# Kernel tuning notes

Hardware: AMD Instinct MI355X
Metric: run time of the kernel (lower is better)

## Reference

```python
import math
import jax, jax.numpy as jnp
import numpy as np

B, T, C, H = 4, 2048, 1024, 16
HD = C // H

def gelu_tanh(x):
    return 0.5 * x * (1.0 + jnp.tanh(jnp.sqrt(2.0 / jnp.pi) * (x + 0.044715 * x * x * x)))

def layernorm(x, w, b, eps=1e-5):
    mu = jnp.mean(x, axis=-1, keepdims=True)
    var = jnp.var(x, axis=-1, keepdims=True)
    return (x - mu) * jax.lax.rsqrt(var + eps) * w + b

def setup_inputs() -> dict:
    key = jax.random.key(0)
    ks = jax.random.split(key, 8)
    s = 0.02
    return {
        "x": jax.random.normal(ks[0], (B, T, C), dtype=jnp.float32),
        "ln1_w": jnp.ones((C,), jnp.float32), "ln1_b": jnp.zeros((C,), jnp.float32),
        "attn_w": jax.random.normal(ks[1], (C, 3 * C), jnp.float32) * s,
        "attn_b": jnp.zeros((3 * C,), jnp.float32),
        "proj_w": jax.random.normal(ks[2], (C, C), jnp.float32) * s,
        "proj_b": jnp.zeros((C,), jnp.float32),
        "ln2_w": jnp.ones((C,), jnp.float32), "ln2_b": jnp.zeros((C,), jnp.float32),
        "fc_w": jax.random.normal(ks[3], (C, 4 * C), jnp.float32) * s,
        "fc_b": jnp.zeros((4 * C,), jnp.float32),
        "fc_proj_w": jax.random.normal(ks[4], (4 * C, C), jnp.float32) * s,
        "fc_proj_b": jnp.zeros((C,), jnp.float32),
    }

def block(x, ln1_w, ln1_b, attn_w, attn_b, proj_w, proj_b,
          ln2_w, ln2_b, fc_w, fc_b, fc_proj_w, fc_proj_b):
    # --- causal self-attention ---
    h = layernorm(x, ln1_w, ln1_b)
    qkv = h @ attn_w + attn_b                      # [B,T,3C]
    q, k, v = jnp.split(qkv, 3, axis=-1)
    q = q.reshape(B, T, H, HD).transpose(0, 2, 1, 3)  # [B,H,T,hd]
    k = k.reshape(B, T, H, HD).transpose(0, 2, 1, 3)
    v = v.reshape(B, T, H, HD).transpose(0, 2, 1, 3)
    att = jnp.einsum('bhqd,bhkd->bhqk', q, k) * (1.0 / math.sqrt(HD))
    mask = jnp.tril(jnp.ones((T, T), dtype=bool))
    att = jnp.where(mask, att, -jnp.inf)
    att = jax.nn.softmax(att, axis=-1)
    y = jnp.einsum('bhqk,bhkd->bhqd', att, v)
    y = y.transpose(0, 2, 1, 3).reshape(B, T, C)
    x = x + (y @ proj_w + proj_b)
    # --- MLP ---
    h = layernorm(x, ln2_w, ln2_b)
    h = gelu_tanh(h @ fc_w + fc_b)
    x = x + (h @ fc_proj_w + fc_proj_b)
    return x

def reference(x, ln1_w, ln1_b, attn_w, attn_b, proj_w, proj_b,
              ln2_w, ln2_b, fc_w, fc_b, fc_proj_w, fc_proj_b):
    return block(x, ln1_w, ln1_b, attn_w, attn_b, proj_w, proj_b,
                 ln2_w, ln2_b, fc_w, fc_b, fc_proj_w, fc_proj_b)
```

## Files before the change

### kernel.cpp

```cpp
#include <hip/hip_runtime.h>
#include <stdint.h>

#define TSEQ 2048
#define CDIM 1024
#define NHEAD 16
#define HDIM 64
#define NROWS 8192

typedef __bf16 bf16x8 __attribute__((ext_vector_type(8)));
typedef float f32x4 __attribute__((ext_vector_type(4)));
typedef float f32x16 __attribute__((ext_vector_type(16)));

__device__ __forceinline__ unsigned short f2bf(float f) {
  unsigned u = __builtin_bit_cast(unsigned, f);
  u = u + 0x7fffu + ((u >> 16) & 1u);
  return (unsigned short)(u >> 16);
}

__device__ __forceinline__ unsigned cvt_pk_bf16(float a, float b) {
  unsigned r;
  asm("v_cvt_pk_bf16_f32 %0, %1, %2" : "=v"(r) : "v"(a), "v"(b));
  return r;
}

__device__ __forceinline__ float gelu_f(float x) {
  float x3 = x * x * x;
  float z = 0.7978845608028654f * (x + 0.044715f * x3);
  float e = __expf(2.f * z);
  float t = 1.f - 2.f / (e + 1.f);
  return 0.5f * x * (1.f + t);
}

__device__ __forceinline__ void ldg_lds16(void* lds, const void* gsrc) {
  __builtin_amdgcn_global_load_lds(
      (__attribute__((address_space(1))) unsigned int*)(uintptr_t)gsrc,
      (__attribute__((address_space(3))) unsigned int*)lds,
      16, 0, 0);
}

__global__ __launch_bounds__(256) void k_wtrans(const float* __restrict__ W,
                                                unsigned short* __restrict__ Wt,
                                                int K, int N) {
  __shared__ unsigned short tl[32][40];
  int n0 = blockIdx.x * 32, k0 = blockIdx.y * 32;
  int tid = threadIdx.x;
  int r = tid >> 3, c4 = (tid & 7) * 4;
  float4 v = *(const float4*)(W + (size_t)(k0 + r) * N + n0 + c4);
  ushort4 o;
  o.x = f2bf(v.x); o.y = f2bf(v.y); o.z = f2bf(v.z); o.w = f2bf(v.w);
  *(ushort4*)&tl[r][c4] = o;
  __syncthreads();
  int n = tid >> 3, k4 = (tid & 7) * 4;
  ushort4 w;
  w.x = tl[k4 + 0][n]; w.y = tl[k4 + 1][n]; w.z = tl[k4 + 2][n]; w.w = tl[k4 + 3][n];
  *(ushort4*)(Wt + (size_t)(n0 + n) * K + k0 + k4) = w;
}

__global__ __launch_bounds__(256) void k_ln(const float* __restrict__ x,
                                            const float* __restrict__ w,
                                            const float* __restrict__ b,
                                            unsigned short* __restrict__ out) {
  int row = blockIdx.x;
  int tid = threadIdx.x;
  const float* xr = x + (size_t)row * CDIM;
  float4 v = *(const float4*)(xr + tid * 4);
  float s = v.x + v.y + v.z + v.w;
  float s2 = v.x * v.x + v.y * v.y + v.z * v.z + v.w * v.w;
#pragma unroll
  for (int off = 32; off; off >>= 1) {
    s += __shfl_xor(s, off);
    s2 += __shfl_xor(s2, off);
  }
  __shared__ float rbuf[8];
  int wv = tid >> 6, lane = tid & 63;
  if (lane == 0) { rbuf[wv] = s; rbuf[4 + wv] = s2; }
  __syncthreads();
  float S1 = rbuf[0] + rbuf[1] + rbuf[2] + rbuf[3];
  float S2 = rbuf[4] + rbuf[5] + rbuf[6] + rbuf[7];
  float mean = S1 * (1.f / CDIM);
  float var = S2 * (1.f / CDIM) - mean * mean;
  float rstd = rsqrtf(var + 1e-5f);
  float4 wv4 = *(const float4*)(w + tid * 4);
  float4 bv4 = *(const float4*)(b + tid * 4);
  ushort4 o;
  o.x = f2bf((v.x - mean) * rstd * wv4.x + bv4.x);
  o.y = f2bf((v.y - mean) * rstd * wv4.y + bv4.y);
  o.z = f2bf((v.z - mean) * rstd * wv4.z + bv4.z);
  o.w = f2bf((v.w - mean) * rstd * wv4.w + bv4.w);
  *(ushort4*)(out + (size_t)row * CDIM + tid * 4) = o;
}

template <int EPI>
__global__ __launch_bounds__(512, 2)
void k_gemm8(const unsigned short* __restrict__ A,
             const unsigned short* __restrict__ Bt,
             const float* __restrict__ bias,
             const float* __restrict__ resid,
             void* __restrict__ Cout,
             int M, int N, int K) {
  __shared__ __align__(16) unsigned short lds[4 * 12288];
  const int tid = threadIdx.x;
  const int wid = tid >> 6, lane = tid & 63;
  const int wm = wid >> 2, wn = wid & 3;
  const int fr = lane & 15, fq = lane >> 4;

  const int gx = gridDim.x;
  int flat = blockIdx.y * gx + blockIdx.x;
  {
    const int nwg = gx * gridDim.y;
    int q = nwg >> 3, r = nwg & 7;
    int xcd = flat & 7, idx = flat >> 3;
    flat = (xcd < r ? xcd * (q + 1) : r * (q + 1) + (xcd - r) * q) + idx;
  }
  const int bx = flat % gx, by = flat / gx;
  const long brow = (long)by * 128, bcol = (long)bx * 256;

  const int sby = (((lane & 3) ^ ((lane >> 3) & 3)) << 4);
  const char* gA = (const char*)(A + ((size_t)(brow + wid * 16 + (lane >> 2))) * K) + sby;
  const char* gB = (const char*)(Bt + ((size_t)(bcol + wid * 32 + (lane >> 2))) * K) + sby;

  const int NT = K >> 5;

#define STAGE_A(t, bf_)                                                 \
  ldg_lds16((char*)lds + (bf_) * 24576 + wid * 1024,                    \
            gA + (size_t)(t) * 64)
#define STAGE_B(i, t, bf_)                                              \
  ldg_lds16((char*)lds + (bf_) * 24576 + 8192 + (wid * 2 + (i)) * 1024, \
            gB + (size_t)(i) * 16 * K * 2 + (size_t)(t) * 64)

  STAGE_A(0, 0); STAGE_B(0, 0, 0); STAGE_B(1, 0, 0);
  STAGE_A(1, 1); STAGE_B(0, 1, 1); STAGE_B(1, 1, 1);
  STAGE_A(2, 2); STAGE_B(0, 2, 2); STAGE_B(1, 2, 2);

  f32x4 acc[4][4];
  const f32x4 vzero = {0.f, 0.f, 0.f, 0.f};
#pragma unroll
  for (int m = 0; m < 4; ++m)
#pragma unroll
    for (int n = 0; n < 4; ++n) acc[m][n] = vzero;

  const int ksw = ((fq ^ ((fr >> 1) & 3)) << 4);
  for (int t = 0; t < NT; ++t) {
    if (t + 2 < NT) asm volatile("s_waitcnt vmcnt(6)" ::: "memory");
    else            asm volatile("s_waitcnt vmcnt(0)" ::: "memory");
    __builtin_amdgcn_s_barrier();
    __builtin_amdgcn_sched_barrier(0);
    const int buf = t & 3, nbuf = (t + 3) & 3;
    if (t + 3 < NT) {
      STAGE_A(t + 3, nbuf); STAGE_B(0, t + 3, nbuf); STAGE_B(1, t + 3, nbuf);
    }
    const char* pA = (const char*)lds + buf * 24576;
    const char* pB = pA + 8192;
    bf16x8 af[4], bfr[4];
#pragma unroll
    for (int m = 0; m < 4; ++m)
      af[m] = *(const bf16x8*)(pA + (wm * 64 + m * 16 + fr) * 64 + ksw);
#pragma unroll
    for (int n = 0; n < 4; ++n)
      bfr[n] = *(const bf16x8*)(pB + (wn * 64 + n * 16 + fr) * 64 + ksw);
    __builtin_amdgcn_s_setprio(1);
#pragma unroll
    for (int m = 0; m < 4; ++m)
#pragma unroll
      for (int n = 0; n < 4; ++n)
        acc[m][n] = __builtin_amdgcn_mfma_f32_16x16x32_bf16(af[m], bfr[n], acc[m][n], 0, 0, 0);
    __builtin_amdgcn_s_setprio(0);
    __builtin_amdgcn_sched_barrier(0);
  }
#undef STAGE_A
#undef STAGE_B

#pragma unroll
  for (int m = 0; m < 4; ++m) {
    long row = brow + wm * 64 + m * 16 + fq * 4;
#pragma unroll
    for (int n = 0; n < 4; ++n) {
      long col = bcol + wn * 64 + n * 16 + fr;
      float bv = bias[col];
#pragma unroll
      for (int r = 0; r < 4; ++r) {
        float v = acc[m][n][r] + bv;
        long idx = (row + r) * (long)N + col;
        if (EPI == 0) {
          ((unsigned short*)Cout)[idx] = f2bf(v);
        } else if (EPI == 1) {
          ((unsigned short*)Cout)[idx] = f2bf(gelu_f(v));
        } else {
          ((float*)Cout)[idx] = v + resid[idx];
        }
      }
    }
  }
}

__global__ __launch_bounds__(256) void k_build_vt(const unsigned short* __restrict__ qkv,
                                                  unsigned short* __restrict__ vt) {
  __shared__ __align__(16) unsigned short tl[64][80];
  int bh = blockIdx.x, b = bh >> 4, h = bh & 15;
  int t0 = blockIdx.y * 64;
  int tid = threadIdx.x;
  int r = tid >> 2, cb = (tid & 3) * 16;
  const unsigned short* src =
      qkv + (size_t)(b * TSEQ + t0 + r) * (3 * CDIM) + 2 * CDIM + h * HDIM + cb;
  *(uint4*)&tl[r][cb] = *(const uint4*)src;
  *(uint4*)&tl[r][cb + 8] = *(const uint4*)(src + 8);
  __syncthreads();
  int d = tid >> 2, tb = (tid & 3) * 16;
  union { unsigned short u[16]; uint4 v[2]; } o;
#pragma unroll
  for (int j = 0; j < 16; ++j) o.u[j] = tl[tb + j][d];
  unsigned short* dst = vt + ((size_t)bh * HDIM + d) * TSEQ + t0 + tb;
  *(uint4*)dst = o.v[0];
  *(uint4*)(dst + 8) = o.v[1];
}

struct QSt {
  f32x16 OTlo, OThi;
  float m, l;
};

__device__ __forceinline__ void attn_qk_sm_pv(
    const bf16x8& k0, const bf16x8& k1, const bf16x8& k2, const bf16x8& k3,
    const bf16x8& v0, const bf16x8& v1, const bf16x8& v2, const bf16x8& v3,
    const bf16x8& q0f, const bf16x8& q1f, const bf16x8& q2f, const bf16x8& q3f,
    QSt& S, bool diag, int lq, int hi) {
  const float SC = 0.125f * 1.44269504088896f;
  f32x16 st;
#pragma unroll
  for (int r = 0; r < 16; ++r) st[r] = 0.f;
  st = __builtin_amdgcn_mfma_f32_32x32x16_bf16(k0, q0f, st, 0, 0, 0);
  st = __builtin_amdgcn_mfma_f32_32x32x16_bf16(k1, q1f, st, 0, 0, 0);
  st = __builtin_amdgcn_mfma_f32_32x32x16_bf16(k2, q2f, st, 0, 0, 0);
  st = __builtin_amdgcn_mfma_f32_32x32x16_bf16(k3, q3f, st, 0, 0, 0);
#pragma unroll
  for (int r = 0; r < 16; ++r) st[r] *= SC;
  if (diag) {
#pragma unroll
    for (int r = 0; r < 16; ++r) {
      int kvl = (r & 3) + 8 * (r >> 2) + 4 * hi;
      if (kvl > lq) st[r] = -1e30f;
    }
  }
  float tmax = st[0];
#pragma unroll
  for (int r = 1; r < 16; ++r) tmax = fmaxf(tmax, st[r]);
  float tm = fmaxf(tmax, __shfl_xor(tmax, 32));
  if (__any(tm > S.m + 8.f)) {
    float mnew = fmaxf(S.m, tm);
    float alpha = __builtin_amdgcn_exp2f(S.m - mnew);
    S.m = mnew;
    S.OTlo *= alpha;
    S.OThi *= alpha;
    S.l *= alpha;
  }
  unsigned c[8];
  float rs = 0.f;
#pragma unroll
  for (int i = 0; i < 8; ++i) {
    float pa = __builtin_amdgcn_exp2f(st[2 * i] - S.m);
    float pb = __builtin_amdgcn_exp2f(st[2 * i + 1] - S.m);
    rs += pa + pb;
    c[i] = cvt_pk_bf16(pa, pb);
  }
  S.l += rs + __shfl_xor(rs, 32);
  unsigned pc[8];
#pragma unroll
  for (int i = 0; i < 8; ++i) pc[i] = __shfl_xor(c[i], 32);
  uint4 w1, w2;
  w1.x = hi ? pc[2] : c[0]; w1.y = hi ? pc[3] : c[1];
  w1.z = hi ? c[2] : pc[0]; w1.w = hi ? c[3] : pc[1];
  w2.x = hi ? pc[6] : c[4]; w2.y = hi ? pc[7] : c[5];
  w2.z = hi ? c[6] : pc[4]; w2.w = hi ? c[7] : pc[5];
  bf16x8 f1 = __builtin_bit_cast(bf16x8, w1);
  bf16x8 f2 = __builtin_bit_cast(bf16x8, w2);
  S.OTlo = __builtin_amdgcn_mfma_f32_32x32x16_bf16(v0, f1, S.OTlo, 0, 0, 0);
  S.OTlo = __builtin_amdgcn_mfma_f32_32x32x16_bf16(v1, f2, S.OTlo, 0, 0, 0);
  S.OThi = __builtin_amdgcn_mfma_f32_32x32x16_bf16(v2, f1, S.OThi, 0, 0, 0);
  S.OThi = __builtin_amdgcn_mfma_f32_32x32x16_bf16(v3, f2, S.OThi, 0, 0, 0);
}

__global__ __launch_bounds__(256, 2) void k_attn(const unsigned short* __restrict__ qkv,
                                                 const unsigned short* __restrict__ vt,
                                                 unsigned short* __restrict__ y) {
  __shared__ __align__(16) unsigned short Ks[2][2048];
  __shared__ __align__(16) unsigned short Vs[2][2048];
  const int bh = blockIdx.x, b = bh >> 4, h = bh & 15;
  const int wv = threadIdx.x >> 6, lane = threadIdx.x & 63;
  const int by = blockIdx.y;
  const int w = by * 4 + wv;
  const int lq = lane & 31, hi = lane >> 5;
  const int ntL = w, ntH = 63 - w;
  const int q0L = w * 32, q0H = (63 - w) * 32;
  const int T = 64 - 4 * by;

  const unsigned short* qrowL = qkv + ((size_t)(b * TSEQ) + q0L + lq) * (3 * CDIM) + h * HDIM;
  const unsigned short* qrowH = qkv + ((size_t)(b * TSEQ) + q0H + lq) * (3 * CDIM) + h * HDIM;
  bf16x8 qL0 = *(const bf16x8*)(qrowL + 0 + hi * 8);
  bf16x8 qL1 = *(const bf16x8*)(qrowL + 16 + hi * 8);
  bf16x8 qL2 = *(const bf16x8*)(qrowL + 32 + hi * 8);
  bf16x8 qL3 = *(const bf16x8*)(qrowL + 48 + hi * 8);
  bf16x8 qH0 = *(const bf16x8*)(qrowH + 0 + hi * 8);
  bf16x8 qH1 = *(const bf16x8*)(qrowH + 16 + hi * 8);
  bf16x8 qH2 = *(const bf16x8*)(qrowH + 32 + hi * 8);
  bf16x8 qH3 = *(const bf16x8*)(qrowH + 48 + hi * 8);

  const int kr = lane & 31, kc = wv * 2 + (lane >> 5);
  const unsigned short* gK =
      qkv + ((size_t)(b * TSEQ) + kr) * (3 * CDIM) + CDIM + h * HDIM + kc * 8;
  const unsigned short* gV = vt + ((size_t)bh * HDIM + lane) * TSEQ + wv * 8;

#define STAGEKV(bf_, tt)                                                  \
  do {                                                                    \
    ldg_lds16((char*)Ks[bf_] + wv * 1024, gK + (size_t)(tt) * 32 * (3 * CDIM)); \
    ldg_lds16((char*)Vs[bf_] + wv * 1024, gV + (tt) * 32);                \
  } while (0)

  QSt SL, SH;
#pragma unroll
  for (int r = 0; r < 16; ++r) {
    SL.OTlo[r] = 0.f; SL.OThi[r] = 0.f; SH.OTlo[r] = 0.f; SH.OThi[r] = 0.f;
  }
  SL.m = -1e30f; SL.l = 0.f; SH.m = -1e30f; SH.l = 0.f;

  STAGEKV(0, 0);
  for (int t = 0; t < T; ++t) {
    __syncthreads();
    if (t + 1 < T) STAGEKV((t + 1) & 1, t + 1);
    if (t <= ntH) {
      const unsigned short* Kb = Ks[t & 1];
      const unsigned short* Vb = Vs[t & 1];
      bf16x8 k0 = *(const bf16x8*)(Kb + (0 + hi) * 256 + lq * 8);
      bf16x8 k1 = *(const bf16x8*)(Kb + (2 + hi) * 256 + lq * 8);
      bf16x8 k2 = *(const bf16x8*)(Kb + (4 + hi) * 256 + lq * 8);
      bf16x8 k3 = *(const bf16x8*)(Kb + (6 + hi) * 256 + lq * 8);
      bf16x8 v0 = *(const bf16x8*)(Vb + hi * 512 + lq * 8);
      bf16x8 v1 = *(const bf16x8*)(Vb + (2 + hi) * 512 + lq * 8);
      bf16x8 v2 = *(const bf16x8*)(Vb + hi * 512 + (lq + 32) * 8);
      bf16x8 v3 = *(const bf16x8*)(Vb + (2 + hi) * 512 + (lq + 32) * 8);
      attn_qk_sm_pv(k0, k1, k2, k3, v0, v1, v2, v3,
                    qH0, qH1, qH2, qH3, SH, t == ntH, lq, hi);
      if (t <= ntL)
        attn_qk_sm_pv(k0, k1, k2, k3, v0, v1, v2, v3,
                      qL0, qL1, qL2, qL3, SL, t == ntL, lq, hi);
    }
  }
#undef STAGEKV

  {
    float inv = 1.f / SH.l;
    unsigned short* yrow = y + ((size_t)(b * TSEQ) + q0H + lq) * CDIM + h * HDIM;
#pragma unroll
    for (int r = 0; r < 16; r += 2) {
      int d = (r & 3) + 8 * (r >> 2) + 4 * hi;
      unsigned lo0 = f2bf(SH.OTlo[r] * inv), lo1 = f2bf(SH.OTlo[r + 1] * inv);
      *(unsigned*)(yrow + d) = lo0 | (lo1 << 16);
      unsigned h0 = f2bf(SH.OThi[r] * inv), h1 = f2bf(SH.OThi[r + 1] * inv);
      *(unsigned*)(yrow + 32 + d) = h0 | (h1 << 16);
    }
  }
  {
    float inv = 1.f / SL.l;
    unsigned short* yrow = y + ((size_t)(b * TSEQ) + q0L + lq) * CDIM + h * HDIM;
#pragma unroll
    for (int r = 0; r < 16; r += 2) {
      int d = (r & 3) + 8 * (r >> 2) + 4 * hi;
      unsigned lo0 = f2bf(SL.OTlo[r] * inv), lo1 = f2bf(SL.OTlo[r + 1] * inv);
      *(unsigned*)(yrow + d) = lo0 | (lo1 << 16);
      unsigned h0 = f2bf(SL.OThi[r] * inv), h1 = f2bf(SL.OThi[r + 1] * inv);
      *(unsigned*)(yrow + 32 + d) = h0 | (h1 << 16);
    }
  }
}

extern "C" void kernel_launch(void* const* d_in, const int* in_sizes, int n_in,
                              void* d_out, int out_size, void* d_ws, size_t ws_size,
                              hipStream_t stream) {
  const float* x = (const float*)d_in[0];
  const float* ln1_w = (const float*)d_in[1];
  const float* ln1_b = (const float*)d_in[2];
  const float* attn_w = (const float*)d_in[3];
  const float* attn_b = (const float*)d_in[4];
  const float* proj_w = (const float*)d_in[5];
  const float* proj_b = (const float*)d_in[6];
  const float* ln2_w = (const float*)d_in[7];
  const float* ln2_b = (const float*)d_in[8];
  const float* fc_w = (const float*)d_in[9];
  const float* fc_b = (const float*)d_in[10];
  const float* fc_proj_w = (const float*)d_in[11];
  const float* fc_proj_b = (const float*)d_in[12];

  char* ws = (char*)d_ws;
  unsigned short* wt_attn = (unsigned short*)(ws + 0);
  unsigned short* wt_proj = (unsigned short*)(ws + 6291456);
  unsigned short* wt_fc = (unsigned short*)(ws + 8388608);
  unsigned short* wt_fcp = (unsigned short*)(ws + 16777216);
  float* x1 = (float*)(ws + 25165824);
  unsigned short* hbuf = (unsigned short*)(ws + 58720256);
  unsigned short* ybuf = (unsigned short*)(ws + 75497472);
  unsigned short* qkvb = (unsigned short*)(ws + 92274688);
  unsigned short* vtb = (unsigned short*)(ws + 142606336);
  unsigned short* gbuf = (unsigned short*)(ws + 92274688);

  k_wtrans<<<dim3(3072 / 32, 1024 / 32), 256, 0, stream>>>(attn_w, wt_attn, 1024, 3072);
  k_wtrans<<<dim3(1024 / 32, 1024 / 32), 256, 0, stream>>>(proj_w, wt_proj, 1024, 1024);
  k_wtrans<<<dim3(4096 / 32, 1024 / 32), 256, 0, stream>>>(fc_w, wt_fc, 1024, 4096);
  k_wtrans<<<dim3(1024 / 32, 4096 / 32), 256, 0, stream>>>(fc_proj_w, wt_fcp, 4096, 1024);

  k_ln<<<NROWS, 256, 0, stream>>>(x, ln1_w, ln1_b, hbuf);

  k_gemm8<0><<<dim3(3072 / 256, NROWS / 128), 512, 0, stream>>>(
      hbuf, wt_attn, attn_b, nullptr, qkvb, NROWS, 3072, 1024);

  k_build_vt<<<dim3(64, TSEQ / 64), 256, 0, stream>>>(qkvb, vtb);

  k_attn<<<dim3(64, 8), 256, 0, stream>>>(qkvb, vtb, ybuf);

  k_gemm8<2><<<dim3(1024 / 256, NROWS / 128), 512, 0, stream>>>(
      ybuf, wt_proj, proj_b, x, x1, NROWS, 1024, 1024);

  k_ln<<<NROWS, 256, 0, stream>>>(x1, ln2_w, ln2_b, hbuf);

  k_gemm8<1><<<dim3(4096 / 256, NROWS / 128), 512, 0, stream>>>(
      hbuf, wt_fc, fc_b, nullptr, gbuf, NROWS, 4096, 1024);

  k_gemm8<2><<<dim3(1024 / 256, NROWS / 128), 512, 0, stream>>>(
      gbuf, wt_fcp, fc_proj_b, x1, (float*)d_out, NROWS, 1024, 4096);
}
```

Before: 387.8 us.

## Template GEMM tile shapes and switch to double-buffered split-phase pipeline

Turns the bf16 MFMA GEMM into a template over warp layout and per-warp fragment counts. The QKV and FC GEMMs now use 256x256 tiles with 8x4 fragments per wave, and the two projection GEMMs use 256x128 tiles. The 4-deep LDS ring is replaced by a 2-buffer scheme whose next-tile loads are issued in the middle of the MFMA phases, and the 8-fragment variant splits its compute into two halves separated by barriers. Larger tiles are meant to raise data reuse per global load, but they cost more registers, add barriers and leave less prefetch depth. The launch bounds claim four blocks per CU, which may not fit in registers.

```diff
diff --git a/kernel.cpp b/kernel.cpp
--- a/kernel.cpp
+++ b/kernel.cpp
@@ -90,18 +90,24 @@
   *(ushort4*)(out + (size_t)row * CDIM + tid * 4) = o;
 }
 
-template <int EPI>
-__global__ __launch_bounds__(512, 2)
-void k_gemm8(const unsigned short* __restrict__ A,
-             const unsigned short* __restrict__ Bt,
-             const float* __restrict__ bias,
-             const float* __restrict__ resid,
-             void* __restrict__ Cout,
-             int M, int N, int K) {
-  __shared__ __align__(16) unsigned short lds[4 * 12288];
+template <int EPI, int WM_, int WN_, int MFR, int NFR>
+__global__ __launch_bounds__(512, 4)
+void k_gemm(const unsigned short* __restrict__ A,
+            const unsigned short* __restrict__ Bt,
+            const float* __restrict__ bias,
+            const float* __restrict__ resid,
+            void* __restrict__ Cout,
+            int M, int N, int K) {
+  constexpr int BM = WM_ * MFR * 16;
+  constexpr int BN = WN_ * NFR * 16;
+  constexpr int ABYTES = BM * 64;
+  constexpr int BBYTES = BN * 64;
+  constexpr int BUFSZ = ABYTES + BBYTES;
+  constexpr int BROWS = BN / 8;
+  __shared__ __align__(16) char lds[2 * BUFSZ];
   const int tid = threadIdx.x;
   const int wid = tid >> 6, lane = tid & 63;
-  const int wm = wid >> 2, wn = wid & 3;
+  const int wm = wid / WN_, wn = wid % WN_;
   const int fr = lane & 15, fq = lane >> 4;
 
   const int gx = gridDim.x;
@@ -113,69 +119,93 @@
     flat = (xcd < r ? xcd * (q + 1) : r * (q + 1) + (xcd - r) * q) + idx;
   }
   const int bx = flat % gx, by = flat / gx;
-  const long brow = (long)by * 128, bcol = (long)bx * 256;
+  const long brow = (long)by * BM, bcol = (long)bx * BN;
 
   const int sby = (((lane & 3) ^ ((lane >> 3) & 3)) << 4);
-  const char* gA = (const char*)(A + ((size_t)(brow + wid * 16 + (lane >> 2))) * K) + sby;
-  const char* gB = (const char*)(Bt + ((size_t)(bcol + wid * 32 + (lane >> 2))) * K) + sby;
+  const char* gA = (const char*)(A + (size_t)(brow + wid * 32 + (lane >> 2)) * K) + sby;
+  const char* gB = (const char*)(Bt + (size_t)(bcol + wid * BROWS + (lane >> 2)) * K) + sby;
 
   const int NT = K >> 5;
 
-#define STAGE_A(t, bf_)                                                 \
-  ldg_lds16((char*)lds + (bf_) * 24576 + wid * 1024,                    \
-            gA + (size_t)(t) * 64)
-#define STAGE_B(i, t, bf_)                                              \
-  ldg_lds16((char*)lds + (bf_) * 24576 + 8192 + (wid * 2 + (i)) * 1024, \
-            gB + (size_t)(i) * 16 * K * 2 + (size_t)(t) * 64)
-
-  STAGE_A(0, 0); STAGE_B(0, 0, 0); STAGE_B(1, 0, 0);
-  STAGE_A(1, 1); STAGE_B(0, 1, 1); STAGE_B(1, 1, 1);
-  STAGE_A(2, 2); STAGE_B(0, 2, 2); STAGE_B(1, 2, 2);
-
-  f32x4 acc[4][4];
+#define STAGE_A(tt, bf)                                                 \
+  do {                                                                  \
+    char* d_ = lds + (bf) * BUFSZ + wid * 2048;                         \
+    ldg_lds16(d_, gA + (size_t)(tt) * 64);                              \
+    ldg_lds16(d_ + 1024, gA + (size_t)16 * K * 2 + (size_t)(tt) * 64);  \
+  } while (0)
+#define STAGE_B(tt, bf)                                                 \
+  do {                                                                  \
+    char* d_ = lds + (bf) * BUFSZ + ABYTES + wid * (BROWS * 64);        \
+    ldg_lds16(d_, gB + (size_t)(tt) * 64);                              \
+    if (BROWS == 32)                                                    \
+      ldg_lds16(d_ + 1024, gB + (size_t)16 * K * 2 + (size_t)(tt) * 64);\
+  } while (0)
+
+  f32x4 acc[MFR][NFR];
   const f32x4 vzero = {0.f, 0.f, 0.f, 0.f};
 #pragma unroll
-  for (int m = 0; m < 4; ++m)
-#pragma unroll
-    for (int n = 0; n < 4; ++n) acc[m][n] = vzero;
+  for (int m = 0; m < MFR; ++m)
+#pragma unroll
+    for (int n = 0; n < NFR; ++n) acc[m][n] = vzero;
+
+  STAGE_A(0, 0); STAGE_B(0, 0);
+  asm volatile("s_waitcnt vmcnt(0)" ::: "memory");
+  __builtin_amdgcn_s_barrier();
 
   const int ksw = ((fq ^ ((fr >> 1) & 3)) << 4);
   for (int t = 0; t < NT; ++t) {
-    if (t + 2 < NT) asm volatile("s_waitcnt vmcnt(6)" ::: "memory");
-    else            asm volatile("s_waitcnt vmcnt(0)" ::: "memory");
+    const bool pre = (t + 1 < NT);
+    const char* pA = lds + (t & 1) * BUFSZ;
+    const char* pB = pA + ABYTES;
+    const int nb = (t & 1) ^ 1;
+    constexpr int M1 = (MFR == 8) ? 4 : MFR;
+    bf16x8 bfr[NFR], a0[M1];
+#pragma unroll
+    for (int n = 0; n < NFR; ++n)
+      bfr[n] = *(const bf16x8*)(pB + (wn * (NFR * 16) + n * 16 + fr) * 64 + ksw);
+#pragma unroll
+    for (int m = 0; m < M1; ++m)
+      a0[m] = *(const bf16x8*)(pA + (wm * (MFR * 16) + m * 16 + fr) * 64 + ksw);
+    if (pre) STAGE_A(t + 1, nb);
+    if (MFR == 4 && pre) STAGE_B(t + 1, nb);
     __builtin_amdgcn_s_barrier();
-    __builtin_amdgcn_sched_barrier(0);
-    const int buf = t & 3, nbuf = (t + 3) & 3;
-    if (t + 3 < NT) {
-      STAGE_A(t + 3, nbuf); STAGE_B(0, t + 3, nbuf); STAGE_B(1, t + 3, nbuf);
-    }
-    const char* pA = (const char*)lds + buf * 24576;
-    const char* pB = pA + 8192;
-    bf16x8 af[4], bfr[4];
-#pragma unroll
-    for (int m = 0; m < 4; ++m)
-      af[m] = *(const bf16x8*)(pA + (wm * 64 + m * 16 + fr) * 64 + ksw);
-#pragma unroll
-    for (int n = 0; n < 4; ++n)
-      bfr[n] = *(const bf16x8*)(pB + (wn * 64 + n * 16 + fr) * 64 + ksw);
+    asm volatile("s_waitcnt lgkmcnt(0)" ::: "memory");
     __builtin_amdgcn_s_setprio(1);
 #pragma unroll
-    for (int m = 0; m < 4; ++m)
-#pragma unroll
-      for (int n = 0; n < 4; ++n)
-        acc[m][n] = __builtin_amdgcn_mfma_f32_16x16x32_bf16(af[m], bfr[n], acc[m][n], 0, 0, 0);
+    for (int m = 0; m < M1; ++m)
+#pragma unroll
+      for (int n = 0; n < NFR; ++n)
+        acc[m][n] = __builtin_amdgcn_mfma_f32_16x16x32_bf16(a0[m], bfr[n], acc[m][n], 0, 0, 0);
     __builtin_amdgcn_s_setprio(0);
-    __builtin_amdgcn_sched_barrier(0);
+    if (MFR == 8) {
+      __builtin_amdgcn_s_barrier();
+      bf16x8 a1[4];
+#pragma unroll
+      for (int m = 0; m < 4; ++m)
+        a1[m] = *(const bf16x8*)(pA + (wm * (MFR * 16) + (m + 4) * 16 + fr) * 64 + ksw);
+      if (pre) STAGE_B(t + 1, nb);
+      __builtin_amdgcn_s_barrier();
+      asm volatile("s_waitcnt lgkmcnt(0)" ::: "memory");
+      __builtin_amdgcn_s_setprio(1);
+#pragma unroll
+      for (int m = 0; m < 4; ++m)
+#pragma unroll
+        for (int n = 0; n < NFR; ++n)
+          acc[m + 4][n] = __builtin_amdgcn_mfma_f32_16x16x32_bf16(a1[m], bfr[n], acc[m + 4][n], 0, 0, 0);
+      __builtin_amdgcn_s_setprio(0);
+    }
+    asm volatile("s_waitcnt vmcnt(0)" ::: "memory");
+    __builtin_amdgcn_s_barrier();
   }
 #undef STAGE_A
 #undef STAGE_B
 
 #pragma unroll
-  for (int m = 0; m < 4; ++m) {
-    long row = brow + wm * 64 + m * 16 + fq * 4;
-#pragma unroll
-    for (int n = 0; n < 4; ++n) {
-      long col = bcol + wn * 64 + n * 16 + fr;
+  for (int m = 0; m < MFR; ++m) {
+    long row = brow + wm * (MFR * 16) + m * 16 + fq * 4;
+#pragma unroll
+    for (int n = 0; n < NFR; ++n) {
+      long col = bcol + wn * (NFR * 16) + n * 16 + fr;
       float bv = bias[col];
 #pragma unroll
       for (int r = 0; r < 4; ++r) {
@@ -408,21 +438,21 @@
 
   k_ln<<<NROWS, 256, 0, stream>>>(x, ln1_w, ln1_b, hbuf);
 
-  k_gemm8<0><<<dim3(3072 / 256, NROWS / 128), 512, 0, stream>>>(
+  k_gemm<0, 2, 4, 8, 4><<<dim3(3072 / 256, NROWS / 256), 512, 0, stream>>>(
       hbuf, wt_attn, attn_b, nullptr, qkvb, NROWS, 3072, 1024);
 
   k_build_vt<<<dim3(64, TSEQ / 64), 256, 0, stream>>>(qkvb, vtb);
 
   k_attn<<<dim3(64, 8), 256, 0, stream>>>(qkvb, vtb, ybuf);
 
-  k_gemm8<2><<<dim3(1024 / 256, NROWS / 128), 512, 0, stream>>>(
+  k_gemm<2, 4, 2, 4, 4><<<dim3(1024 / 128, NROWS / 256), 512, 0, stream>>>(
       ybuf, wt_proj, proj_b, x, x1, NROWS, 1024, 1024);
 
   k_ln<<<NROWS, 256, 0, stream>>>(x1, ln2_w, ln2_b, hbuf);
 
-  k_gemm8<1><<<dim3(4096 / 256, NROWS / 128), 512, 0, stream>>>(
+  k_gemm<1, 2, 4, 8, 4><<<dim3(4096 / 256, NROWS / 256), 512, 0, stream>>>(
       hbuf, wt_fc, fc_b, nullptr, gbuf, NROWS, 4096, 1024);
 
-  k_gemm8<2><<<dim3(1024 / 256, NROWS / 128), 512, 0, stream>>>(
+  k_gemm<2, 4, 2, 4, 4><<<dim3(1024 / 128, NROWS / 256), 512, 0, stream>>>(
       gbuf, wt_fcp, fc_proj_b, x1, (float*)d_out, NROWS, 1024, 4096);
 }
```

New measurement: 1.351 ms. 3.48x slower.
